# Performance work log

Hardware: AMD Instinct MI355X
Metric: run time of the kernel (lower is better)

Reference implementation:

```python
import jax, jax.numpy as jnp
import numpy as np

V, D, H, P = 30000, 2048, 512, 196  # vocab, encoder_dim, hidden, num pixels


def setup_inputs() -> dict:
    key = jax.random.key(0)
    ks = jax.random.split(key, 16)
    s = 0.02
    inp = {
        'img_features': jax.random.normal(ks[0], (32, P, D), jnp.float32),
        'captions': jax.random.randint(ks[1], (32, 20), 0, V),
        # LSTMCell: gates order i,f,g,o; weights stored [in, 4H]
        'Wih': jax.random.normal(ks[2], (H + D, 4 * H), jnp.float32) * s,
        'Whh': jax.random.normal(ks[3], (H, 4 * H), jnp.float32) * s,
        'bih': jnp.zeros((4 * H,), jnp.float32),
        'bhh': jnp.zeros((4 * H,), jnp.float32),
        'W_init_h': jax.random.normal(ks[4], (D, H), jnp.float32) * s,
        'b_init_h': jnp.zeros((H,), jnp.float32),
        'W_init_c': jax.random.normal(ks[5], (D, H), jnp.float32) * s,
        'b_init_c': jnp.zeros((H,), jnp.float32),
        'W_fbeta': jax.random.normal(ks[6], (H, D), jnp.float32) * s,
        'b_fbeta': jnp.zeros((D,), jnp.float32),
        'W_out': jax.random.normal(ks[7], (H, V), jnp.float32) * s,
        'b_out': jnp.zeros((V,), jnp.float32),
        'W_att_img': jax.random.normal(ks[8], (D, H), jnp.float32) * s,
        'b_att_img': jnp.zeros((H,), jnp.float32),
        'W_att_h': jax.random.normal(ks[9], (H, H), jnp.float32) * s,
        'b_att_h': jnp.zeros((H,), jnp.float32),
        'v_att': jax.random.normal(ks[10], (H, 1), jnp.float32) * s,
        'b_v_att': jnp.zeros((1,), jnp.float32),
        'E': jax.random.normal(ks[11], (V, H), jnp.float32) * s,
    }
    return inp


def reference(img_features, captions, Wih, Whh, bih, bhh, W_init_h, b_init_h,
              W_init_c, b_init_c, W_fbeta, b_fbeta, W_out, b_out,
              W_att_img, b_att_img, W_att_h, b_att_h, v_att, b_v_att, E):
    # init LSTM state from mean pooled image features
    avg = img_features.mean(axis=1)                      # [B,D]
    h0 = jnp.tanh(avg @ W_init_h + b_init_h)             # [B,H]
    c0 = jnp.tanh(avg @ W_init_c + b_init_c)
    att_img = img_features @ W_att_img + b_att_img       # [B,P,H] precomputed
    emb = E[captions]                                    # [B,T,H]
    T = captions.shape[1] - 1                            # max_timespan

    def step(carry, emb_t):
        h, c = carry
        # soft attention
        att = jnp.tanh(att_img + (h @ W_att_h + b_att_h)[:, None, :])  # [B,P,H]
        e = jnp.squeeze(att @ v_att, -1) + b_v_att                     # [B,P]
        alpha = jax.nn.softmax(e, axis=-1)
        context = jnp.einsum('bp,bpd->bd', alpha, img_features)        # [B,D]
        gate = jax.nn.sigmoid(h @ W_fbeta + b_fbeta)                   # [B,D]
        x = jnp.concatenate([emb_t, gate * context], axis=1)           # [B,H+D]
        gates = x @ Wih + h @ Whh + bih + bhh                          # [B,4H]
        i, f, g, o = jnp.split(gates, 4, axis=1)
        c = jax.nn.sigmoid(f) * c + jax.nn.sigmoid(i) * jnp.tanh(g)
        h = jax.nn.sigmoid(o) * jnp.tanh(c)
        out = h @ W_out + b_out                                        # [B,V] (dropout=identity)
        return (h, c), (out, alpha)

    emb_t = jnp.swapaxes(emb[:, :T], 0, 1)               # [T,B,H]
    _, (preds, alphas) = jax.lax.scan(step, (h0, c0), emb_t)
    preds = jnp.swapaxes(preds, 0, 1)                    # [B,T,V]
    alphas = jnp.swapaxes(alphas, 0, 1)                  # [B,T,P]
    return preds, alphas
```

## Files before the change

### kernel.cpp

```cpp
#include <hip/hip_runtime.h>
#include <hip/hip_bf16.h>

#define BB_ 32
#define PP_ 196
#define DD_ 2048
#define HH_ 512
#define VV_ 30000
#define TT_ 19
#define KX_ 2560
#define KG_ 3072
#define NTV_ 1875
#define NBOUT_ 469

typedef __attribute__((ext_vector_type(8))) short bf16x8;
typedef __attribute__((ext_vector_type(4))) float f32x4;

__device__ __forceinline__ unsigned short bf16b(float x) {
    __hip_bfloat16 h = __float2bfloat16(x);
    unsigned short u; __builtin_memcpy(&u, &h, 2); return u;
}
__device__ __forceinline__ float b2f(unsigned short u) {
    return __uint_as_float((unsigned int)u << 16);
}
__device__ __forceinline__ float sigf(float x) { return 1.f / (1.f + __expf(-x)); }
__device__ __forceinline__ float ftanh(float x) {
    return 1.f - 2.f / (__expf(2.f * x) + 1.f);
}


__device__ __forceinline__ void d_cvt8(int bid, int tid,
        const float* __restrict__ src, unsigned short* __restrict__ dst) {
    size_t i0 = ((size_t)bid * 256 + tid) * 8;
    float4 a = *(const float4*)&src[i0];
    float4 b = *(const float4*)&src[i0 + 4];
    bf16x8 v;
    v[0]=bf16b(a.x); v[1]=bf16b(a.y); v[2]=bf16b(a.z); v[3]=bf16b(a.w);
    v[4]=bf16b(b.x); v[5]=bf16b(b.y); v[6]=bf16b(b.z); v[7]=bf16b(b.w);
    *(bf16x8*)&dst[i0] = v;
}

__device__ __forceinline__ void d_nsplit(int bid, int tid,
        const float* __restrict__ A, int NA, const float* __restrict__ Bp, int NB,
        int K, unsigned short* __restrict__ dst) {
    int gid = bid * 256 + tid;
    int lane = gid & 63, rest = gid >> 6;
    int KS = K >> 5;
    int ks = rest % KS, nt = rest / KS;
    int g = lane >> 4, r = lane & 15;
    int k0 = ks * 32 + g * 8;
    int n = nt * 16 + r;
    const float* src; int stride, col;
    if (n < NA) { src = A; stride = NA; col = n; }
    else        { src = Bp; stride = NB; col = n - NA; }
    bf16x8 v;
#pragma unroll
    for (int i = 0; i < 8; i++)
        v[i] = bf16b(src[(size_t)(k0 + i) * stride + col]);
    *(bf16x8*)&dst[(size_t)gid * 8] = v;
}

__device__ __forceinline__ void d_ksplit(int bid, int tid,
        const float* __restrict__ A, int KA, const float* __restrict__ Bp,
        int K, int N, unsigned short* __restrict__ dst) {
    int gid = bid * 256 + tid;
    int lane = gid & 63, rest = gid >> 6;
    int KS = K >> 5;
    int ks = rest % KS, nt = rest / KS;
    int g = lane >> 4, r = lane & 15;
    int k0 = ks * 32 + g * 8;
    int n = nt * 16 + r;
    bf16x8 v;
#pragma unroll
    for (int i = 0; i < 8; i++) {
        int k = k0 + i;
        const float* src = (k < KA) ? &A[(size_t)k * N] : &Bp[(size_t)(k - KA) * N];
        v[i] = bf16b(src[n]);
    }
    *(bf16x8*)&dst[(size_t)gid * 8] = v;
}

__global__ __launch_bounds__(256) void k_cvt_all(
        const float* __restrict__ img, unsigned short* __restrict__ imgb,
        const float* __restrict__ Wout, unsigned short* __restrict__ wof,
        const float* __restrict__ Wai, unsigned short* __restrict__ waf,
        const float* __restrict__ Wah, const float* __restrict__ Wfb,
        unsigned short* __restrict__ whf,
        const float* __restrict__ Wih, const float* __restrict__ Whh,
        unsigned short* __restrict__ wgf,
        const float* __restrict__ Winh, const float* __restrict__ Winc,
        unsigned short* __restrict__ wif) {
    int b = blockIdx.x, t = threadIdx.x;
    if (b < 6272)       d_cvt8(b, t, img, imgb);
    else if (b < 13772) d_nsplit(b - 6272, t, Wout, VV_, Wout, 0, HH_, wof);
    else if (b < 14284) d_nsplit(b - 13772, t, Wai, HH_, Wai, 0, DD_, waf);
    else if (b < 14924) d_nsplit(b - 14284, t, Wah, HH_, Wfb, DD_, HH_, whf);
    else if (b < 17996) d_ksplit(b - 14924, t, Wih, KX_, Whh, KG_, 2048, wgf);
    else                d_nsplit(b - 17996, t, Winh, HH_, Winc, HH_, DD_, wif);
}


__global__ __launch_bounds__(256) void k_meanpool(const float* __restrict__ img,
                                                  unsigned short* __restrict__ avgb) {
    int b = blockIdx.x, tid = threadIdx.x;
    int d0 = tid * 8;
    const float* p = img + (size_t)b * PP_ * DD_ + d0;
    float s[8] = {};
    for (int i = 0; i < PP_; i++) {
        float4 a = *(const float4*)&p[(size_t)i * DD_];
        float4 c = *(const float4*)&p[(size_t)i * DD_ + 4];
        s[0]+=a.x; s[1]+=a.y; s[2]+=a.z; s[3]+=a.w;
        s[4]+=c.x; s[5]+=c.y; s[6]+=c.z; s[7]+=c.w;
    }
    bf16x8 v;
#pragma unroll
    for (int i = 0; i < 8; i++) v[i] = bf16b(s[i] * (1.0f / PP_));
    *(bf16x8*)&avgb[b * DD_ + d0] = v;
}

__global__ __launch_bounds__(256) void k_init_mfma(const unsigned short* __restrict__ avgb,
        const unsigned short* __restrict__ wif, const float* __restrict__ binh,
        const float* __restrict__ binc, float* __restrict__ c,
        unsigned short* __restrict__ hb) {
    int wid = blockIdx.x * 4 + (threadIdx.x >> 6);
    int lane = threadIdx.x & 63;
    int g = lane >> 4, r = lane & 15;
    f32x4 acc[2] = {};
    const unsigned short* a_base = avgb + (size_t)r * DD_ + g * 8;
#pragma unroll 4
    for (int ks = 0; ks < DD_ / 32; ks++) {
        bf16x8 a0 = *(const bf16x8*)(a_base + ks * 32);
        bf16x8 a1 = *(const bf16x8*)(a_base + 16 * DD_ + ks * 32);
        bf16x8 bf = *(const bf16x8*)(wif + ((size_t)(wid * 64 + ks) * 64 + lane) * 8);
        acc[0] = __builtin_amdgcn_mfma_f32_16x16x32_bf16(a0, bf, acc[0], 0, 0, 0);
        acc[1] = __builtin_amdgcn_mfma_f32_16x16x32_bf16(a1, bf, acc[1], 0, 0, 0);
    }
    int n = wid * 16 + r;
#pragma unroll
    for (int a = 0; a < 2; a++)
#pragma unroll
        for (int j = 0; j < 4; j++) {
            int m = 16 * a + 4 * g + j;
            float v = ftanh(acc[a][j] + ((n < HH_) ? binh[n] : binc[n - HH_]));
            if (n < HH_) hb[m * HH_ + n] = bf16b(v);
            else c[m * HH_ + (n - HH_)] = v;
        }
}

__global__ __launch_bounds__(256) void k_attimg_mfma(const unsigned short* __restrict__ imgb,
        const unsigned short* __restrict__ waf, const float* __restrict__ bias,
        unsigned short* __restrict__ attb) {
    int wid = blockIdx.x * 4 + (threadIdx.x >> 6);
    int lane = threadIdx.x & 63;
    int g = lane >> 4, r = lane & 15;
    int mblk = wid >> 4, nblk = wid & 15;
    int m0 = mblk * 32, nt0 = nblk * 2;
    f32x4 acc[2][2] = {};
    const unsigned short* a_base = imgb + (size_t)(m0 + r) * DD_ + g * 8;
#pragma unroll 4
    for (int ks = 0; ks < DD_ / 32; ks++) {
        bf16x8 a0 = *(const bf16x8*)(a_base + ks * 32);
        bf16x8 a1 = *(const bf16x8*)(a_base + 16 * DD_ + ks * 32);
        bf16x8 b0 = *(const bf16x8*)(waf + ((size_t)((nt0 + 0) * 64 + ks) * 64 + lane) * 8);
        bf16x8 b1 = *(const bf16x8*)(waf + ((size_t)((nt0 + 1) * 64 + ks) * 64 + lane) * 8);
        acc[0][0] = __builtin_amdgcn_mfma_f32_16x16x32_bf16(a0, b0, acc[0][0], 0, 0, 0);
        acc[0][1] = __builtin_amdgcn_mfma_f32_16x16x32_bf16(a0, b1, acc[0][1], 0, 0, 0);
        acc[1][0] = __builtin_amdgcn_mfma_f32_16x16x32_bf16(a1, b0, acc[1][0], 0, 0, 0);
        acc[1][1] = __builtin_amdgcn_mfma_f32_16x16x32_bf16(a1, b1, acc[1][1], 0, 0, 0);
    }
#pragma unroll
    for (int mi = 0; mi < 2; mi++)
#pragma unroll
        for (int ni = 0; ni < 2; ni++) {
            int n = (nt0 + ni) * 16 + r;
            float bn = bias[n];
#pragma unroll
            for (int j = 0; j < 4; j++) {
                int m = m0 + 16 * mi + 4 * g + j;
                attb[(size_t)m * HH_ + n] = bf16b(acc[mi][ni][j] + bn);
            }
        }
}


__device__ __forceinline__ void hmats_body(int wid, int lane,
        const unsigned short* __restrict__ hb, const unsigned short* __restrict__ whf,
        const float* __restrict__ bah, const float* __restrict__ bfb,
        float* __restrict__ hWatt, float* __restrict__ gate) {
    int g = lane >> 4, r = lane & 15;
    f32x4 acc[2] = {};
    const unsigned short* a_base = hb + (size_t)r * HH_ + g * 8;
#pragma unroll
    for (int ks = 0; ks < HH_ / 32; ks++) {
        bf16x8 a0 = *(const bf16x8*)(a_base + ks * 32);
        bf16x8 a1 = *(const bf16x8*)(a_base + 16 * HH_ + ks * 32);
        bf16x8 bf = *(const bf16x8*)(whf + ((size_t)(wid * 16 + ks) * 64 + lane) * 8);
        acc[0] = __builtin_amdgcn_mfma_f32_16x16x32_bf16(a0, bf, acc[0], 0, 0, 0);
        acc[1] = __builtin_amdgcn_mfma_f32_16x16x32_bf16(a1, bf, acc[1], 0, 0, 0);
    }
    int n = wid * 16 + r;
#pragma unroll
    for (int a = 0; a < 2; a++)
#pragma unroll
        for (int j = 0; j < 4; j++) {
            int m = 16 * a + 4 * g + j;
            float v = acc[a][j];
            if (n < HH_) hWatt[m * HH_ + n] = v + bah[n];
            else gate[m * DD_ + (n - HH_)] = sigf(v + bfb[n - HH_]);
        }
}

__global__ __launch_bounds__(256) void k_hmats_mfma(const unsigned short* __restrict__ hb,
        const unsigned short* __restrict__ whf, const float* __restrict__ bah,
        const float* __restrict__ bfb, float* __restrict__ hWatt, float* __restrict__ gate) {
    int wid = blockIdx.x * 4 + (threadIdx.x >> 6);
    hmats_body(wid, threadIdx.x & 63, hb, whf, bah, bfb, hWatt, gate);
}

__global__ __launch_bounds__(256) void k_step1(const unsigned short* __restrict__ attb,
        const unsigned short* __restrict__ imgb, const float* __restrict__ hWatt,
        const float* __restrict__ gate, const float* __restrict__ Emb,
        const int* __restrict__ captions, const float* __restrict__ v_att,
        const float* __restrict__ b_v, int t, unsigned short* __restrict__ xhb,
        const unsigned short* __restrict__ hb, float* __restrict__ alpha_out) {
    __shared__ float e_lds[PP_];
    __shared__ float sa[PP_];
    __shared__ float red[256];
    const int b = blockIdx.x, dc = blockIdx.y, tid = threadIdx.x;
    const int wv = tid >> 6, lane = tid & 63;
    const float* hw = hWatt + (size_t)b * HH_ + lane * 8;
    float hw8[8], vv8[8];
    {
        float4 h0 = *(const float4*)&hw[0];
        float4 h1 = *(const float4*)&hw[4];
        const float* vp = v_att + lane * 8;
        float4 v0 = *(const float4*)&vp[0];
        float4 v1 = *(const float4*)&vp[4];
        hw8[0]=h0.x; hw8[1]=h0.y; hw8[2]=h0.z; hw8[3]=h0.w;
        hw8[4]=h1.x; hw8[5]=h1.y; hw8[6]=h1.z; hw8[7]=h1.w;
        vv8[0]=v0.x; vv8[1]=v0.y; vv8[2]=v0.z; vv8[3]=v0.w;
        vv8[4]=v1.x; vv8[5]=v1.y; vv8[6]=v1.z; vv8[7]=v1.w;
    }
    float bv0 = b_v[0];
    const unsigned short* ab = attb + (size_t)b * PP_ * HH_ + lane * 8;
    for (int i = 0; i < 49; i++) {
        int p = wv * 49 + i;
        bf16x8 av = *(const bf16x8*)(ab + (size_t)p * HH_);
        float acc = 0.f;
#pragma unroll
        for (int j = 0; j < 8; j++)
            acc += vv8[j] * ftanh(b2f((unsigned short)av[j]) + hw8[j]);
        for (int off = 32; off > 0; off >>= 1) acc += __shfl_down(acc, off);
        if (lane == 0) e_lds[p] = acc + bv0;
    }
    __syncthreads();
    float ev = (tid < PP_) ? e_lds[tid] : -1e30f;
    red[tid] = ev;
    __syncthreads();
    for (int s = 128; s > 0; s >>= 1) {
        if (tid < s) red[tid] = fmaxf(red[tid], red[tid + s]);
        __syncthreads();
    }
    float mx = red[0];
    __syncthreads();
    float pv = (tid < PP_) ? __expf(ev - mx) : 0.f;
    red[tid] = pv;
    __syncthreads();
    for (int s = 128; s > 0; s >>= 1) {
        if (tid < s) red[tid] += red[tid + s];
        __syncthreads();
    }
    float inv = 1.f / red[0];
    if (tid < PP_) sa[tid] = pv * inv;
    __syncthreads();
    int d0 = dc * 1024 + tid * 4;
    const unsigned short* ib = imgb + (size_t)b * PP_ * DD_ + d0;
    float a0 = 0.f, a1 = 0.f, a2 = 0.f, a3 = 0.f;
#pragma unroll 4
    for (int p = 0; p < PP_; p++) {
        uint2 v = *(const uint2*)&ib[(size_t)p * DD_];
        float s = sa[p];
        a0 += s * __uint_as_float(v.x << 16);
        a1 += s * __uint_as_float(v.x & 0xffff0000u);
        a2 += s * __uint_as_float(v.y << 16);
        a3 += s * __uint_as_float(v.y & 0xffff0000u);
    }
    float4 gv = *(const float4*)&gate[b * DD_ + d0];
    unsigned int u01 = (unsigned int)bf16b(gv.x * a0) | ((unsigned int)bf16b(gv.y * a1) << 16);
    unsigned int u23 = (unsigned int)bf16b(gv.z * a2) | ((unsigned int)bf16b(gv.w * a3) << 16);
    *(uint2*)&xhb[b * KG_ + HH_ + d0] = make_uint2(u01, u23);
    if (dc == 0) {
        if (tid < PP_) alpha_out[((size_t)b * TT_ + t) * PP_ + tid] = sa[tid];
        if (tid < 128) {
            int tok = captions[b * 20 + t];
            float4 evec = *(const float4*)&Emb[(size_t)tok * HH_ + tid * 4];
            unsigned int e01 = (unsigned int)bf16b(evec.x) | ((unsigned int)bf16b(evec.y) << 16);
            unsigned int e23 = (unsigned int)bf16b(evec.z) | ((unsigned int)bf16b(evec.w) << 16);
            *(uint2*)&xhb[b * KG_ + tid * 4] = make_uint2(e01, e23);
        } else {
            int i = tid - 128;
            *(uint2*)&xhb[b * KG_ + KX_ + i * 4] = *(const uint2*)&hb[b * HH_ + i * 4];
        }
    }
}

__global__ __launch_bounds__(1024) void k_gateslstm(const unsigned short* __restrict__ xhb,
        const unsigned short* __restrict__ wgf, const float* __restrict__ bih,
        const float* __restrict__ bhh, float* __restrict__ c,
        unsigned short* __restrict__ hb) {
    __shared__ float part[16][BB_][16];
    __shared__ float gsum[4][BB_][16];
    const int tid = threadIdx.x;
    const int w = tid >> 6, lane = tid & 63;
    const int q = w & 3, kc = w >> 2;
    const int g = lane >> 4, r = lane & 15;
    const int jb = blockIdx.x;
    const int nt = q * 32 + jb;
    f32x4 acc[2] = {};
    const unsigned short* a_base = xhb + (size_t)r * KG_ + g * 8;
#pragma unroll 4
    for (int i = 0; i < 24; i++) {
        int ks = kc * 24 + i;
        bf16x8 a0 = *(const bf16x8*)(a_base + ks * 32);
        bf16x8 a1 = *(const bf16x8*)(a_base + 16 * KG_ + ks * 32);
        bf16x8 bf = *(const bf16x8*)(wgf + ((size_t)(nt * 96 + ks) * 64 + lane) * 8);
        acc[0] = __builtin_amdgcn_mfma_f32_16x16x32_bf16(a0, bf, acc[0], 0, 0, 0);
        acc[1] = __builtin_amdgcn_mfma_f32_16x16x32_bf16(a1, bf, acc[1], 0, 0, 0);
    }
#pragma unroll
    for (int a = 0; a < 2; a++)
#pragma unroll
        for (int j = 0; j < 4; j++)
            part[w][16 * a + 4 * g + j][r] = acc[a][j];
    __syncthreads();
    {
        int qq = tid >> 8, s2 = tid & 255;
        int m = s2 >> 3, j0 = (s2 & 7) * 2;
#pragma unroll
        for (int jj = 0; jj < 2; jj++) {
            int jc = j0 + jj;
            gsum[qq][m][jc] = part[qq][m][jc] + part[4 + qq][m][jc]
                            + part[8 + qq][m][jc] + part[12 + qq][m][jc];
        }
    }
    __syncthreads();
    if (tid < 512) {
        int m = tid >> 4, jc = tid & 15;
        int jg = jb * 16 + jc;
        float gi = gsum[0][m][jc] + bih[jg] + bhh[jg];
        float gf = gsum[1][m][jc] + bih[HH_ + jg] + bhh[HH_ + jg];
        float gg = gsum[2][m][jc] + bih[2 * HH_ + jg] + bhh[2 * HH_ + jg];
        float go = gsum[3][m][jc] + bih[3 * HH_ + jg] + bhh[3 * HH_ + jg];
        int ci = m * HH_ + jg;
        float cn = sigf(gf) * c[ci] + sigf(gi) * ftanh(gg);
        float hn = sigf(go) * ftanh(cn);
        c[ci] = cn;
        hb[ci] = bf16b(hn);
    }
}

__global__ __launch_bounds__(256) void k_out_hmats(const unsigned short* __restrict__ hb,
        const unsigned short* __restrict__ wof, const float* __restrict__ bout,
        const unsigned short* __restrict__ whf, const float* __restrict__ bah,
        const float* __restrict__ bfb, float* __restrict__ preds,
        float* __restrict__ hWatt, float* __restrict__ gate, int t) {
    int lane = threadIdx.x & 63;
    int wv = threadIdx.x >> 6;
    if (blockIdx.x >= NBOUT_) {
        int wid = (blockIdx.x - NBOUT_) * 4 + wv;
        hmats_body(wid, lane, hb, whf, bah, bfb, hWatt, gate);
        return;
    }
    int nt = blockIdx.x * 4 + wv;
    if (nt >= NTV_) return;
    int g = lane >> 4, r = lane & 15;
    f32x4 acc[2] = {};
    const unsigned short* a_base = hb + (size_t)r * HH_ + g * 8;
#pragma unroll
    for (int ks = 0; ks < HH_ / 32; ks++) {
        bf16x8 a0 = *(const bf16x8*)(a_base + ks * 32);
        bf16x8 a1 = *(const bf16x8*)(a_base + 16 * HH_ + ks * 32);
        bf16x8 bf = *(const bf16x8*)(wof + ((size_t)(nt * 16 + ks) * 64 + lane) * 8);
        acc[0] = __builtin_amdgcn_mfma_f32_16x16x32_bf16(a0, bf, acc[0], 0, 0, 0);
        acc[1] = __builtin_amdgcn_mfma_f32_16x16x32_bf16(a1, bf, acc[1], 0, 0, 0);
    }
    int n = nt * 16 + r;
    float bn = bout[n];
#pragma unroll
    for (int a = 0; a < 2; a++)
#pragma unroll
        for (int j = 0; j < 4; j++) {
            int m = 16 * a + 4 * g + j;
            preds[((size_t)m * TT_ + t) * VV_ + n] = acc[a][j] + bn;
        }
}


extern "C" void kernel_launch(void* const* d_in, const int* in_sizes, int n_in,
                              void* d_out, int out_size, void* d_ws, size_t ws_size,
                              hipStream_t stream) {
    const float* img     = (const float*)d_in[0];
    const int*   caps    = (const int*)d_in[1];
    const float* Wih     = (const float*)d_in[2];
    const float* Whh     = (const float*)d_in[3];
    const float* bih     = (const float*)d_in[4];
    const float* bhh     = (const float*)d_in[5];
    const float* Winh    = (const float*)d_in[6];
    const float* binh    = (const float*)d_in[7];
    const float* Winc    = (const float*)d_in[8];
    const float* binc    = (const float*)d_in[9];
    const float* Wfb     = (const float*)d_in[10];
    const float* bfb     = (const float*)d_in[11];
    const float* Wout    = (const float*)d_in[12];
    const float* bout    = (const float*)d_in[13];
    const float* Wai     = (const float*)d_in[14];
    const float* bai     = (const float*)d_in[15];
    const float* Wah     = (const float*)d_in[16];
    const float* bah     = (const float*)d_in[17];
    const float* v_att   = (const float*)d_in[18];
    const float* b_v     = (const float*)d_in[19];
    const float* Emb     = (const float*)d_in[20];

    float* preds  = (float*)d_out;
    float* alphas = (float*)d_out + (size_t)BB_ * TT_ * VV_;

    char* w = (char*)d_ws;
    size_t off = 0;
    auto alloc = [&](size_t bytes) {
        char* p = w + off;
        off += (bytes + 255) & ~(size_t)255;
        return p;
    };
    unsigned short* imgb = (unsigned short*)alloc((size_t)BB_ * PP_ * DD_ * 2);
    unsigned short* wof  = (unsigned short*)alloc((size_t)HH_ * VV_ * 2);
    unsigned short* wgf  = (unsigned short*)alloc((size_t)KG_ * 2048 * 2);
    unsigned short* waf  = (unsigned short*)alloc((size_t)DD_ * HH_ * 2);
    unsigned short* whf  = (unsigned short*)alloc((size_t)HH_ * KX_ * 2);
    unsigned short* wif  = (unsigned short*)alloc((size_t)DD_ * 1024 * 2);
    unsigned short* attb = (unsigned short*)alloc((size_t)BB_ * PP_ * HH_ * 2);
    unsigned short* avgb = (unsigned short*)alloc((size_t)BB_ * DD_ * 2);
    float* c       = (float*)alloc((size_t)BB_ * HH_ * 4);
    float* hWatt   = (float*)alloc((size_t)BB_ * HH_ * 4);
    float* gate    = (float*)alloc((size_t)BB_ * DD_ * 4);
    unsigned short* hb  = (unsigned short*)alloc((size_t)BB_ * HH_ * 2);
    unsigned short* xhb = (unsigned short*)alloc((size_t)BB_ * KG_ * 2);
    (void)ws_size;

    k_cvt_all<<<19020, 256, 0, stream>>>(img, imgb, Wout, wof, Wai, waf,
                                         Wah, Wfb, whf, Wih, Whh, wgf,
                                         Winh, Winc, wif);
    k_meanpool<<<BB_, 256, 0, stream>>>(img, avgb);
    k_init_mfma<<<16, 256, 0, stream>>>(avgb, wif, binh, binc, c, hb);
    k_attimg_mfma<<<784, 256, 0, stream>>>(imgb, waf, bai, attb);
    k_hmats_mfma<<<40, 256, 0, stream>>>(hb, whf, bah, bfb, hWatt, gate);

    for (int t = 0; t < TT_; t++) {
        k_step1<<<dim3(BB_, 2), 256, 0, stream>>>(attb, imgb, hWatt, gate, Emb,
                                                  caps, v_att, b_v, t, xhb, hb, alphas);
        k_gateslstm<<<BB_, 1024, 0, stream>>>(xhb, wgf, bih, bhh, c, hb);
        k_out_hmats<<<509, 256, 0, stream>>>(hb, wof, bout, whf, bah, bfb,
                                             preds, hWatt, gate, t);
    }
}
```

Measured before the change: 2.228 ms.

## Fuse per-timestep kernels into one persistent kernel with grid barriers

Replaces the 57 per-timestep launches (attention, LSTM gates, output projection) with a single persistent kernel of 240 blocks of 1024 threads. The stages are separated by an atomic grid-wide barrier. This removes launch overhead and gaps between kernels. The attention stage now splits each batch row over 4 blocks, and the attimg GEMM uses larger 64x64 per-wave tiles for more register reuse. The risks are deadlock if the 240 blocks are not all co-resident, barrier latency, and lower per-stage parallelism because only 32 or 128 blocks do work in some phases.

Result: slower. 7.942 ms (+256.5%).

```diff
diff --git a/kernel.cpp b/kernel.cpp
--- a/kernel.cpp
+++ b/kernel.cpp
@@ -9,8 +9,9 @@
 #define TT_ 19
 #define KX_ 2560
 #define KG_ 3072
+#define NBLK_ 240
 #define NTV_ 1875
-#define NBOUT_ 469
+#define NTH_ 160
 
 typedef __attribute__((ext_vector_type(8))) short bf16x8;
 typedef __attribute__((ext_vector_type(4))) float f32x4;
@@ -25,6 +26,27 @@
 __device__ __forceinline__ float sigf(float x) { return 1.f / (1.f + __expf(-x)); }
 __device__ __forceinline__ float ftanh(float x) {
     return 1.f - 2.f / (__expf(2.f * x) + 1.f);
+}
+__device__ __forceinline__ f32x4 mfma16(bf16x8 a, bf16x8 b, f32x4 c) {
+    return __builtin_amdgcn_mfma_f32_16x16x32_bf16(a, b, c, 0, 0, 0);
+}
+
+__device__ __forceinline__ void gbar(unsigned* bar) {
+    __syncthreads();
+    if (threadIdx.x == 0) {
+        __threadfence();
+        unsigned gen = __hip_atomic_load(&bar[1], __ATOMIC_RELAXED, __HIP_MEMORY_SCOPE_AGENT);
+        unsigned arr = __hip_atomic_fetch_add(&bar[0], 1u, __ATOMIC_ACQ_REL, __HIP_MEMORY_SCOPE_AGENT);
+        if (arr == NBLK_ - 1u) {
+            __hip_atomic_store(&bar[0], 0u, __ATOMIC_RELAXED, __HIP_MEMORY_SCOPE_AGENT);
+            __hip_atomic_fetch_add(&bar[1], 1u, __ATOMIC_RELEASE, __HIP_MEMORY_SCOPE_AGENT);
+        } else {
+            while (__hip_atomic_load(&bar[1], __ATOMIC_ACQUIRE, __HIP_MEMORY_SCOPE_AGENT) == gen)
+                __builtin_amdgcn_s_sleep(1);
+        }
+        __threadfence();
+    }
+    __syncthreads();
 }
 
 
@@ -131,8 +153,8 @@
         bf16x8 a0 = *(const bf16x8*)(a_base + ks * 32);
         bf16x8 a1 = *(const bf16x8*)(a_base + 16 * DD_ + ks * 32);
         bf16x8 bf = *(const bf16x8*)(wif + ((size_t)(wid * 64 + ks) * 64 + lane) * 8);
-        acc[0] = __builtin_amdgcn_mfma_f32_16x16x32_bf16(a0, bf, acc[0], 0, 0, 0);
-        acc[1] = __builtin_amdgcn_mfma_f32_16x16x32_bf16(a1, bf, acc[1], 0, 0, 0);
+        acc[0] = mfma16(a0, bf, acc[0]);
+        acc[1] = mfma16(a1, bf, acc[1]);
     }
     int n = wid * 16 + r;
 #pragma unroll
@@ -152,25 +174,28 @@
     int wid = blockIdx.x * 4 + (threadIdx.x >> 6);
     int lane = threadIdx.x & 63;
     int g = lane >> 4, r = lane & 15;
-    int mblk = wid >> 4, nblk = wid & 15;
-    int m0 = mblk * 32, nt0 = nblk * 2;
-    f32x4 acc[2][2] = {};
+    int mt = wid >> 3, ntb = wid & 7;
+    int m0 = mt * 64, nt0 = ntb * 4;
+    f32x4 acc[4][4] = {};
     const unsigned short* a_base = imgb + (size_t)(m0 + r) * DD_ + g * 8;
-#pragma unroll 4
     for (int ks = 0; ks < DD_ / 32; ks++) {
-        bf16x8 a0 = *(const bf16x8*)(a_base + ks * 32);
-        bf16x8 a1 = *(const bf16x8*)(a_base + 16 * DD_ + ks * 32);
-        bf16x8 b0 = *(const bf16x8*)(waf + ((size_t)((nt0 + 0) * 64 + ks) * 64 + lane) * 8);
-        bf16x8 b1 = *(const bf16x8*)(waf + ((size_t)((nt0 + 1) * 64 + ks) * 64 + lane) * 8);
-        acc[0][0] = __builtin_amdgcn_mfma_f32_16x16x32_bf16(a0, b0, acc[0][0], 0, 0, 0);
-        acc[0][1] = __builtin_amdgcn_mfma_f32_16x16x32_bf16(a0, b1, acc[0][1], 0, 0, 0);
-        acc[1][0] = __builtin_amdgcn_mfma_f32_16x16x32_bf16(a1, b0, acc[1][0], 0, 0, 0);
-        acc[1][1] = __builtin_amdgcn_mfma_f32_16x16x32_bf16(a1, b1, acc[1][1], 0, 0, 0);
-    }
-#pragma unroll
-    for (int mi = 0; mi < 2; mi++)
-#pragma unroll
-        for (int ni = 0; ni < 2; ni++) {
+        bf16x8 a[4], b[4];
+#pragma unroll
+        for (int mi = 0; mi < 4; mi++)
+            a[mi] = *(const bf16x8*)(a_base + (size_t)(16 * mi) * DD_ + ks * 32);
+#pragma unroll
+        for (int ni = 0; ni < 4; ni++)
+            b[ni] = *(const bf16x8*)(waf + (((size_t)(nt0 + ni) * 64 + ks) * 64 + lane) * 8);
+#pragma unroll
+        for (int mi = 0; mi < 4; mi++)
+#pragma unroll
+            for (int ni = 0; ni < 4; ni++)
+                acc[mi][ni] = mfma16(a[mi], b[ni], acc[mi][ni]);
+    }
+#pragma unroll
+    for (int mi = 0; mi < 4; mi++)
+#pragma unroll
+        for (int ni = 0; ni < 4; ni++) {
             int n = (nt0 + ni) * 16 + r;
             float bn = bias[n];
 #pragma unroll
@@ -180,7 +205,6 @@
             }
         }
 }
-
 
 __device__ __forceinline__ void hmats_body(int wid, int lane,
         const unsigned short* __restrict__ hb, const unsigned short* __restrict__ whf,
@@ -194,8 +218,8 @@
         bf16x8 a0 = *(const bf16x8*)(a_base + ks * 32);
         bf16x8 a1 = *(const bf16x8*)(a_base + 16 * HH_ + ks * 32);
         bf16x8 bf = *(const bf16x8*)(whf + ((size_t)(wid * 16 + ks) * 64 + lane) * 8);
-        acc[0] = __builtin_amdgcn_mfma_f32_16x16x32_bf16(a0, bf, acc[0], 0, 0, 0);
-        acc[1] = __builtin_amdgcn_mfma_f32_16x16x32_bf16(a1, bf, acc[1], 0, 0, 0);
+        acc[0] = mfma16(a0, bf, acc[0]);
+        acc[1] = mfma16(a1, bf, acc[1]);
     }
     int n = wid * 16 + r;
 #pragma unroll
@@ -209,189 +233,188 @@
         }
 }
 
-__global__ __launch_bounds__(256) void k_hmats_mfma(const unsigned short* __restrict__ hb,
-        const unsigned short* __restrict__ whf, const float* __restrict__ bah,
-        const float* __restrict__ bfb, float* __restrict__ hWatt, float* __restrict__ gate) {
-    int wid = blockIdx.x * 4 + (threadIdx.x >> 6);
-    hmats_body(wid, threadIdx.x & 63, hb, whf, bah, bfb, hWatt, gate);
-}
-
-__global__ __launch_bounds__(256) void k_step1(const unsigned short* __restrict__ attb,
-        const unsigned short* __restrict__ imgb, const float* __restrict__ hWatt,
-        const float* __restrict__ gate, const float* __restrict__ Emb,
-        const int* __restrict__ captions, const float* __restrict__ v_att,
-        const float* __restrict__ b_v, int t, unsigned short* __restrict__ xhb,
-        const unsigned short* __restrict__ hb, float* __restrict__ alpha_out) {
-    __shared__ float e_lds[PP_];
-    __shared__ float sa[PP_];
-    __shared__ float red[256];
-    const int b = blockIdx.x, dc = blockIdx.y, tid = threadIdx.x;
+
+__global__ __launch_bounds__(1024) void k_persist(
+        const unsigned short* __restrict__ attb, const unsigned short* __restrict__ imgb,
+        const unsigned short* __restrict__ wgf, const unsigned short* __restrict__ wof,
+        const unsigned short* __restrict__ whf,
+        const float* __restrict__ bih, const float* __restrict__ bhh,
+        const float* __restrict__ bout, const float* __restrict__ bah,
+        const float* __restrict__ bfb, const float* __restrict__ v_att,
+        const float* __restrict__ b_v, const float* __restrict__ Emb,
+        const int* __restrict__ caps,
+        float* __restrict__ c, unsigned short* __restrict__ hb,
+        unsigned short* __restrict__ xhb, float* __restrict__ hWatt,
+        float* __restrict__ gate, float* __restrict__ preds,
+        float* __restrict__ alphas, unsigned* __restrict__ bar) {
+    __shared__ float s_part[16][BB_][16];
+    __shared__ float s_gsum[4][BB_][16];
+    __shared__ float s_e[PP_];
+    __shared__ float s_sa[PP_];
+    __shared__ float s_red[256];
+    const int tid = threadIdx.x;
     const int wv = tid >> 6, lane = tid & 63;
-    const float* hw = hWatt + (size_t)b * HH_ + lane * 8;
-    float hw8[8], vv8[8];
+    const int g = lane >> 4, r = lane & 15;
+    const int blk = blockIdx.x;
+
     {
-        float4 h0 = *(const float4*)&hw[0];
-        float4 h1 = *(const float4*)&hw[4];
-        const float* vp = v_att + lane * 8;
-        float4 v0 = *(const float4*)&vp[0];
-        float4 v1 = *(const float4*)&vp[4];
-        hw8[0]=h0.x; hw8[1]=h0.y; hw8[2]=h0.z; hw8[3]=h0.w;
-        hw8[4]=h1.x; hw8[5]=h1.y; hw8[6]=h1.z; hw8[7]=h1.w;
-        vv8[0]=v0.x; vv8[1]=v0.y; vv8[2]=v0.z; vv8[3]=v0.w;
-        vv8[4]=v1.x; vv8[5]=v1.y; vv8[6]=v1.z; vv8[7]=v1.w;
-    }
-    float bv0 = b_v[0];
-    const unsigned short* ab = attb + (size_t)b * PP_ * HH_ + lane * 8;
-    for (int i = 0; i < 49; i++) {
-        int p = wv * 49 + i;
-        bf16x8 av = *(const bf16x8*)(ab + (size_t)p * HH_);
-        float acc = 0.f;
-#pragma unroll
-        for (int j = 0; j < 8; j++)
-            acc += vv8[j] * ftanh(b2f((unsigned short)av[j]) + hw8[j]);
-        for (int off = 32; off > 0; off >>= 1) acc += __shfl_down(acc, off);
-        if (lane == 0) e_lds[p] = acc + bv0;
-    }
-    __syncthreads();
-    float ev = (tid < PP_) ? e_lds[tid] : -1e30f;
-    red[tid] = ev;
-    __syncthreads();
-    for (int s = 128; s > 0; s >>= 1) {
-        if (tid < s) red[tid] = fmaxf(red[tid], red[tid + s]);
-        __syncthreads();
-    }
-    float mx = red[0];
-    __syncthreads();
-    float pv = (tid < PP_) ? __expf(ev - mx) : 0.f;
-    red[tid] = pv;
-    __syncthreads();
-    for (int s = 128; s > 0; s >>= 1) {
-        if (tid < s) red[tid] += red[tid + s];
-        __syncthreads();
-    }
-    float inv = 1.f / red[0];
-    if (tid < PP_) sa[tid] = pv * inv;
-    __syncthreads();
-    int d0 = dc * 1024 + tid * 4;
-    const unsigned short* ib = imgb + (size_t)b * PP_ * DD_ + d0;
-    float a0 = 0.f, a1 = 0.f, a2 = 0.f, a3 = 0.f;
+        int wid = blk * 16 + wv;
+        if (wid < NTH_) hmats_body(wid, lane, hb, whf, bah, bfb, hWatt, gate);
+    }
+    gbar(bar);
+
+    for (int t = 0; t < TT_; t++) {
+        if (blk < 128) {
+            const int b = blk >> 2, quarter = blk & 3;
+            {
+                const float* hw = hWatt + (size_t)b * HH_ + lane * 8;
+                float4 h0 = *(const float4*)&hw[0];
+                float4 h1 = *(const float4*)&hw[4];
+                const float* vp = v_att + lane * 8;
+                float4 v0 = *(const float4*)&vp[0];
+                float4 v1 = *(const float4*)&vp[4];
+                float hw8[8] = {h0.x,h0.y,h0.z,h0.w,h1.x,h1.y,h1.z,h1.w};
+                float vv8[8] = {v0.x,v0.y,v0.z,v0.w,v1.x,v1.y,v1.z,v1.w};
+                float bv0 = b_v[0];
+                const unsigned short* ab = attb + (size_t)b * PP_ * HH_ + lane * 8;
+                for (int p = wv; p < PP_; p += 16) {
+                    bf16x8 av = *(const bf16x8*)(ab + (size_t)p * HH_);
+                    float acc = 0.f;
+#pragma unroll
+                    for (int j = 0; j < 8; j++)
+                        acc += vv8[j] * ftanh(b2f((unsigned short)av[j]) + hw8[j]);
+#pragma unroll
+                    for (int off = 32; off > 0; off >>= 1) acc += __shfl_down(acc, off);
+                    if (lane == 0) s_e[p] = acc + bv0;
+                }
+            }
+            __syncthreads();
+            float ev = (tid < PP_) ? s_e[tid] : -1e30f;
+            if (tid < 256) s_red[tid] = ev;
+            __syncthreads();
+            for (int s = 128; s > 0; s >>= 1) {
+                if (tid < s) s_red[tid] = fmaxf(s_red[tid], s_red[tid + s]);
+                __syncthreads();
+            }
+            float mx = s_red[0];
+            __syncthreads();
+            float pv = (tid < PP_) ? __expf(ev - mx) : 0.f;
+            if (tid < 256) s_red[tid] = pv;
+            __syncthreads();
+            for (int s = 128; s > 0; s >>= 1) {
+                if (tid < s) s_red[tid] += s_red[tid + s];
+                __syncthreads();
+            }
+            float inv = 1.f / s_red[0];
+            if (tid < PP_) s_sa[tid] = pv * inv;
+            __syncthreads();
+            if (tid < 256) {
+                int d0 = quarter * 512 + tid * 2;
+                const unsigned short* ib = imgb + (size_t)b * PP_ * DD_ + d0;
+                float a0 = 0.f, a1 = 0.f;
 #pragma unroll 4
-    for (int p = 0; p < PP_; p++) {
-        uint2 v = *(const uint2*)&ib[(size_t)p * DD_];
-        float s = sa[p];
-        a0 += s * __uint_as_float(v.x << 16);
-        a1 += s * __uint_as_float(v.x & 0xffff0000u);
-        a2 += s * __uint_as_float(v.y << 16);
-        a3 += s * __uint_as_float(v.y & 0xffff0000u);
-    }
-    float4 gv = *(const float4*)&gate[b * DD_ + d0];
-    unsigned int u01 = (unsigned int)bf16b(gv.x * a0) | ((unsigned int)bf16b(gv.y * a1) << 16);
-    unsigned int u23 = (unsigned int)bf16b(gv.z * a2) | ((unsigned int)bf16b(gv.w * a3) << 16);
-    *(uint2*)&xhb[b * KG_ + HH_ + d0] = make_uint2(u01, u23);
-    if (dc == 0) {
-        if (tid < PP_) alpha_out[((size_t)b * TT_ + t) * PP_ + tid] = sa[tid];
-        if (tid < 128) {
-            int tok = captions[b * 20 + t];
-            float4 evec = *(const float4*)&Emb[(size_t)tok * HH_ + tid * 4];
-            unsigned int e01 = (unsigned int)bf16b(evec.x) | ((unsigned int)bf16b(evec.y) << 16);
-            unsigned int e23 = (unsigned int)bf16b(evec.z) | ((unsigned int)bf16b(evec.w) << 16);
-            *(uint2*)&xhb[b * KG_ + tid * 4] = make_uint2(e01, e23);
-        } else {
-            int i = tid - 128;
-            *(uint2*)&xhb[b * KG_ + KX_ + i * 4] = *(const uint2*)&hb[b * HH_ + i * 4];
-        }
-    }
-}
-
-__global__ __launch_bounds__(1024) void k_gateslstm(const unsigned short* __restrict__ xhb,
-        const unsigned short* __restrict__ wgf, const float* __restrict__ bih,
-        const float* __restrict__ bhh, float* __restrict__ c,
-        unsigned short* __restrict__ hb) {
-    __shared__ float part[16][BB_][16];
-    __shared__ float gsum[4][BB_][16];
-    const int tid = threadIdx.x;
-    const int w = tid >> 6, lane = tid & 63;
-    const int q = w & 3, kc = w >> 2;
-    const int g = lane >> 4, r = lane & 15;
-    const int jb = blockIdx.x;
-    const int nt = q * 32 + jb;
-    f32x4 acc[2] = {};
-    const unsigned short* a_base = xhb + (size_t)r * KG_ + g * 8;
+                for (int p = 0; p < PP_; p++) {
+                    unsigned int v = *(const unsigned int*)&ib[(size_t)p * DD_];
+                    float s = s_sa[p];
+                    a0 += s * __uint_as_float(v << 16);
+                    a1 += s * __uint_as_float(v & 0xffff0000u);
+                }
+                float2 gv = *(const float2*)&gate[b * DD_ + d0];
+                unsigned int pk = (unsigned int)bf16b(gv.x * a0)
+                                | ((unsigned int)bf16b(gv.y * a1) << 16);
+                *(unsigned int*)&xhb[b * KG_ + HH_ + d0] = pk;
+            } else if (quarter == 0 && tid >= 512) {
+                if (tid < 640) {
+                    int i = tid - 512;
+                    int tok = caps[b * 20 + t];
+                    float4 evec = *(const float4*)&Emb[(size_t)tok * HH_ + i * 4];
+                    unsigned int e01 = (unsigned int)bf16b(evec.x) | ((unsigned int)bf16b(evec.y) << 16);
+                    unsigned int e23 = (unsigned int)bf16b(evec.z) | ((unsigned int)bf16b(evec.w) << 16);
+                    *(uint2*)&xhb[b * KG_ + i * 4] = make_uint2(e01, e23);
+                } else if (tid < 768) {
+                    int i = tid - 640;
+                    *(uint2*)&xhb[b * KG_ + KX_ + i * 4] = *(const uint2*)&hb[b * HH_ + i * 4];
+                } else if (tid < 768 + PP_) {
+                    alphas[((size_t)b * TT_ + t) * PP_ + (tid - 768)] = s_sa[tid - 768];
+                }
+            }
+        }
+        gbar(bar);
+        if (blk < 32) {
+            const int q = wv & 3, kc = wv >> 2;
+            const int jb = blk;
+            const int nt = q * 32 + jb;
+            f32x4 acc[2] = {};
+            const unsigned short* a_base = xhb + (size_t)r * KG_ + g * 8;
 #pragma unroll 4
-    for (int i = 0; i < 24; i++) {
-        int ks = kc * 24 + i;
-        bf16x8 a0 = *(const bf16x8*)(a_base + ks * 32);
-        bf16x8 a1 = *(const bf16x8*)(a_base + 16 * KG_ + ks * 32);
-        bf16x8 bf = *(const bf16x8*)(wgf + ((size_t)(nt * 96 + ks) * 64 + lane) * 8);
-        acc[0] = __builtin_amdgcn_mfma_f32_16x16x32_bf16(a0, bf, acc[0], 0, 0, 0);
-        acc[1] = __builtin_amdgcn_mfma_f32_16x16x32_bf16(a1, bf, acc[1], 0, 0, 0);
-    }
-#pragma unroll
-    for (int a = 0; a < 2; a++)
-#pragma unroll
-        for (int j = 0; j < 4; j++)
-            part[w][16 * a + 4 * g + j][r] = acc[a][j];
-    __syncthreads();
-    {
-        int qq = tid >> 8, s2 = tid & 255;
-        int m = s2 >> 3, j0 = (s2 & 7) * 2;
-#pragma unroll
-        for (int jj = 0; jj < 2; jj++) {
-            int jc = j0 + jj;
-            gsum[qq][m][jc] = part[qq][m][jc] + part[4 + qq][m][jc]
-                            + part[8 + qq][m][jc] + part[12 + qq][m][jc];
-        }
-    }
-    __syncthreads();
-    if (tid < 512) {
-        int m = tid >> 4, jc = tid & 15;
-        int jg = jb * 16 + jc;
-        float gi = gsum[0][m][jc] + bih[jg] + bhh[jg];
-        float gf = gsum[1][m][jc] + bih[HH_ + jg] + bhh[HH_ + jg];
-        float gg = gsum[2][m][jc] + bih[2 * HH_ + jg] + bhh[2 * HH_ + jg];
-        float go = gsum[3][m][jc] + bih[3 * HH_ + jg] + bhh[3 * HH_ + jg];
-        int ci = m * HH_ + jg;
-        float cn = sigf(gf) * c[ci] + sigf(gi) * ftanh(gg);
-        float hn = sigf(go) * ftanh(cn);
-        c[ci] = cn;
-        hb[ci] = bf16b(hn);
-    }
-}
-
-__global__ __launch_bounds__(256) void k_out_hmats(const unsigned short* __restrict__ hb,
-        const unsigned short* __restrict__ wof, const float* __restrict__ bout,
-        const unsigned short* __restrict__ whf, const float* __restrict__ bah,
-        const float* __restrict__ bfb, float* __restrict__ preds,
-        float* __restrict__ hWatt, float* __restrict__ gate, int t) {
-    int lane = threadIdx.x & 63;
-    int wv = threadIdx.x >> 6;
-    if (blockIdx.x >= NBOUT_) {
-        int wid = (blockIdx.x - NBOUT_) * 4 + wv;
-        hmats_body(wid, lane, hb, whf, bah, bfb, hWatt, gate);
-        return;
-    }
-    int nt = blockIdx.x * 4 + wv;
-    if (nt >= NTV_) return;
-    int g = lane >> 4, r = lane & 15;
-    f32x4 acc[2] = {};
-    const unsigned short* a_base = hb + (size_t)r * HH_ + g * 8;
-#pragma unroll
-    for (int ks = 0; ks < HH_ / 32; ks++) {
-        bf16x8 a0 = *(const bf16x8*)(a_base + ks * 32);
-        bf16x8 a1 = *(const bf16x8*)(a_base + 16 * HH_ + ks * 32);
-        bf16x8 bf = *(const bf16x8*)(wof + ((size_t)(nt * 16 + ks) * 64 + lane) * 8);
-        acc[0] = __builtin_amdgcn_mfma_f32_16x16x32_bf16(a0, bf, acc[0], 0, 0, 0);
-        acc[1] = __builtin_amdgcn_mfma_f32_16x16x32_bf16(a1, bf, acc[1], 0, 0, 0);
-    }
-    int n = nt * 16 + r;
-    float bn = bout[n];
-#pragma unroll
-    for (int a = 0; a < 2; a++)
-#pragma unroll
-        for (int j = 0; j < 4; j++) {
-            int m = 16 * a + 4 * g + j;
-            preds[((size_t)m * TT_ + t) * VV_ + n] = acc[a][j] + bn;
-        }
+            for (int i = 0; i < 24; i++) {
+                int ks = kc * 24 + i;
+                bf16x8 a0 = *(const bf16x8*)(a_base + ks * 32);
+                bf16x8 a1 = *(const bf16x8*)(a_base + 16 * KG_ + ks * 32);
+                bf16x8 bf = *(const bf16x8*)(wgf + ((size_t)(nt * 96 + ks) * 64 + lane) * 8);
+                acc[0] = mfma16(a0, bf, acc[0]);
+                acc[1] = mfma16(a1, bf, acc[1]);
+            }
+#pragma unroll
+            for (int a = 0; a < 2; a++)
+#pragma unroll
+                for (int j = 0; j < 4; j++)
+                    s_part[wv][16 * a + 4 * g + j][r] = acc[a][j];
+            __syncthreads();
+            {
+                int qq = tid >> 8, s2 = tid & 255;
+                int m = s2 >> 3, j0 = (s2 & 7) * 2;
+#pragma unroll
+                for (int jj = 0; jj < 2; jj++) {
+                    int jc = j0 + jj;
+                    s_gsum[qq][m][jc] = s_part[qq][m][jc] + s_part[4 + qq][m][jc]
+                                      + s_part[8 + qq][m][jc] + s_part[12 + qq][m][jc];
+                }
+            }
+            __syncthreads();
+            if (tid < 512) {
+                int m = tid >> 4, jc = tid & 15;
+                int jg = jb * 16 + jc;
+                float gi = s_gsum[0][m][jc] + bih[jg] + bhh[jg];
+                float gf = s_gsum[1][m][jc] + bih[HH_ + jg] + bhh[HH_ + jg];
+                float gg = s_gsum[2][m][jc] + bih[2 * HH_ + jg] + bhh[2 * HH_ + jg];
+                float go = s_gsum[3][m][jc] + bih[3 * HH_ + jg] + bhh[3 * HH_ + jg];
+                int ci = m * HH_ + jg;
+                float cn = sigf(gf) * c[ci] + sigf(gi) * ftanh(gg);
+                float hn = sigf(go) * ftanh(cn);
+                c[ci] = cn;
+                hb[ci] = bf16b(hn);
+            }
+        }
+        gbar(bar);
+        {
+            int gwid = blk * 16 + wv;
+            if (gwid < NTV_) {
+                f32x4 acc[2] = {};
+                const unsigned short* a_base = hb + (size_t)r * HH_ + g * 8;
+#pragma unroll
+                for (int ks = 0; ks < HH_ / 32; ks++) {
+                    bf16x8 a0 = *(const bf16x8*)(a_base + ks * 32);
+                    bf16x8 a1 = *(const bf16x8*)(a_base + 16 * HH_ + ks * 32);
+                    bf16x8 bf = *(const bf16x8*)(wof + ((size_t)(gwid * 16 + ks) * 64 + lane) * 8);
+                    acc[0] = mfma16(a0, bf, acc[0]);
+                    acc[1] = mfma16(a1, bf, acc[1]);
+                }
+                int n = gwid * 16 + r;
+                float bn = bout[n];
+#pragma unroll
+                for (int a = 0; a < 2; a++)
+#pragma unroll
+                    for (int j = 0; j < 4; j++) {
+                        int m = 16 * a + 4 * g + j;
+                        preds[((size_t)m * TT_ + t) * VV_ + n] = acc[a][j] + bn;
+                    }
+            } else if (gwid < NTV_ + NTH_) {
+                hmats_body(gwid - NTV_, lane, hb, whf, bah, bfb, hWatt, gate);
+            }
+        }
+        gbar(bar);
+    }
 }
 
 
@@ -443,21 +466,21 @@
     float* gate    = (float*)alloc((size_t)BB_ * DD_ * 4);
     unsigned short* hb  = (unsigned short*)alloc((size_t)BB_ * HH_ * 2);
     unsigned short* xhb = (unsigned short*)alloc((size_t)BB_ * KG_ * 2);
+    unsigned* bar = (unsigned*)alloc(256);
     (void)ws_size;
+
+    hipMemsetAsync(bar, 0, 256, stream);
 
     k_cvt_all<<<19020, 256, 0, stream>>>(img, imgb, Wout, wof, Wai, waf,
                                          Wah, Wfb, whf, Wih, Whh, wgf,
                                          Winh, Winc, wif);
     k_meanpool<<<BB_, 256, 0, stream>>>(img, avgb);
     k_init_mfma<<<16, 256, 0, stream>>>(avgb, wif, binh, binc, c, hb);
-    k_attimg_mfma<<<784, 256, 0, stream>>>(imgb, waf, bai, attb);
-    k_hmats_mfma<<<40, 256, 0, stream>>>(hb, whf, bah, bfb, hWatt, gate);
-
-    for (int t = 0; t < TT_; t++) {
-        k_step1<<<dim3(BB_, 2), 256, 0, stream>>>(attb, imgb, hWatt, gate, Emb,
-                                                  caps, v_att, b_v, t, xhb, hb, alphas);
-        k_gateslstm<<<BB_, 1024, 0, stream>>>(xhb, wgf, bih, bhh, c, hb);
-        k_out_hmats<<<509, 256, 0, stream>>>(hb, wof, bout, whf, bah, bfb,
-                                             preds, hWatt, gate, t);
-    }
-}
+    k_attimg_mfma<<<196, 256, 0, stream>>>(imgb, waf, bai, attb);
+
+    k_persist<<<NBLK_, 1024, 0, stream>>>(attb, imgb, wgf, wof, whf,
+                                          bih, bhh, bout, bah, bfb,
+                                          v_att, b_v, Emb, caps,
+                                          c, hb, xhb, hWatt, gate,
+                                          preds, alphas, bar);
+}
```
